# Kernel optimization log

Measured on AMD Instinct MI355X. Metric: run time of the kernel, lower is better.

The kernel has to match this reference:

```python
import jax, jax.numpy as jnp
import numpy as np

D_MODEL = 2048
N_HEADS = 8
N_KV = 4
HEAD_DIM = 256
WINDOW = 1024
EPS = 1e-6
ROPE_BASE = 10000.0


def _rms_norm(x, w):
    # x: [..., D]; matches torch: x * rsqrt(mean(x^2) + eps) * w
    return x * jax.lax.rsqrt(jnp.mean(x * x, axis=-1, keepdims=True) + EPS) * w


def _rope_cos_sin(pos):
    # pos: [T] ints -> cos/sin: [T, HEAD_DIM] (cat(freqs, freqs) as in source)
    inv_freq = 1.0 / (ROPE_BASE ** (jnp.arange(0, HEAD_DIM, 2, dtype=jnp.float32) / HEAD_DIM))
    freqs = pos.astype(jnp.float32)[:, None] * inv_freq[None, :]  # [T, D/2]
    emb = jnp.concatenate([freqs, freqs], axis=-1)                # [T, D]
    return jnp.cos(emb), jnp.sin(emb)


def _apply_rotary(x, cos, sin):
    # x: [B, H, T, D]; interleaved rotate-half exactly as the torch code
    x1 = x[..., 0::2]
    x2 = x[..., 1::2]
    x_rot = jnp.stack([-x2, x1], axis=-1).reshape(x.shape)
    return x * cos[None, None, :, :] + x_rot * sin[None, None, :, :]


def setup_inputs() -> dict:
    key = jax.random.key(0)
    ks = jax.random.split(key, 8)
    B, T = 1, 4096
    s = 0.02
    return {
        "x": jax.random.normal(ks[0], (B, T, D_MODEL), dtype=jnp.float32),
        "pos": jnp.arange(T, dtype=jnp.int32),
        "Wq": jax.random.normal(ks[1], (N_HEADS * HEAD_DIM, D_MODEL), dtype=jnp.float32) * s,
        "Wk": jax.random.normal(ks[2], (N_KV * HEAD_DIM, D_MODEL), dtype=jnp.float32) * s,
        "Wv": jax.random.normal(ks[3], (N_KV * HEAD_DIM, D_MODEL), dtype=jnp.float32) * s,
        "Wo": jax.random.normal(ks[4], (D_MODEL, N_HEADS * HEAD_DIM), dtype=jnp.float32) * s,
        "q_norm_w": jnp.ones((HEAD_DIM,), dtype=jnp.float32),
        "k_norm_w": jnp.ones((HEAD_DIM,), dtype=jnp.float32),
    }


def reference(x, pos, Wq, Wk, Wv, Wo, q_norm_w, k_norm_w):
    B, T, _ = x.shape
    # projections (torch Linear: y = x @ W.T)
    q = (x @ Wq.T).reshape(B, T, N_HEADS, HEAD_DIM).transpose(0, 2, 1, 3)  # [B,H,T,D]
    k = (x @ Wk.T).reshape(B, T, N_KV, HEAD_DIM).transpose(0, 2, 1, 3)    # [B,Hkv,T,D]
    v = (x @ Wv.T).reshape(B, T, N_KV, HEAD_DIM).transpose(0, 2, 1, 3)
    # per-head RMSNorm
    q = _rms_norm(q, q_norm_w)
    k = _rms_norm(k, k_norm_w)
    # RoPE
    cos, sin = _rope_cos_sin(pos)
    q = _apply_rotary(q, cos, sin)
    k = _apply_rotary(k, cos, sin)
    # GQA repeat: [B,Hkv,T,D] -> [B,H,T,D]
    rep = N_HEADS // N_KV
    k = jnp.repeat(k, rep, axis=1)
    v = jnp.repeat(v, rep, axis=1)
    # full scores + sliding-window causal mask (faithful to source)
    scores = jnp.einsum("bhqd,bhkd->bhqk", q, k) / jnp.sqrt(jnp.float32(HEAD_DIM))
    i = jnp.arange(T)[:, None]
    j = jnp.arange(T)[None, :]
    allowed = (j <= i) & (j >= i - WINDOW + 1)  # [T,T]
    scores = jnp.where(allowed[None, None, :, :], scores, -jnp.inf)
    attn = jax.nn.softmax(scores, axis=-1)
    y = jnp.einsum("bhqk,bhkd->bhqd", attn, v)
    y = y.transpose(0, 2, 1, 3).reshape(B, T, N_HEADS * HEAD_DIM)
    return y @ Wo.T
```

## Files before the change

### kernel.cpp

```cpp
#include <hip/hip_runtime.h>
#include <cstdint>
#include <cmath>

typedef __bf16 bf16x8 __attribute__((ext_vector_type(8)));
typedef float  f32x4  __attribute__((ext_vector_type(4)));

#define DEVI __device__ __forceinline__

#define SEQ 4096
#define NH 8
#define NKV 4
#define HD 256
#define WIN 1024

DEVI void gload16(const void* g, void* l) {
  __builtin_amdgcn_global_load_lds((const __attribute__((address_space(1))) void*)g,
                                   (__attribute__((address_space(3))) void*)l,
                                   16, 0, 0);
}

DEVI bf16x8 ld8f(const float* p) {
  const f32x4 a = *(const f32x4*)p;
  const f32x4 b = *(const f32x4*)(p + 4);
  bf16x8 r;
#pragma unroll
  for (int j = 0; j < 4; ++j) { r[j] = (__bf16)a[j]; r[4 + j] = (__bf16)b[j]; }
  return r;
}

DEVI void st1(float* p, float v)  { *p = v; }
DEVI void st1(__bf16* p, float v) { *p = (__bf16)v; }

DEVI void barx() {
  asm volatile("" ::: "memory");
  __builtin_amdgcn_s_barrier();
  asm volatile("" ::: "memory");
}

__global__ __launch_bounds__(256)
void cvt_all(const float* __restrict__ x,  const float* __restrict__ wq,
             const float* __restrict__ wk, const float* __restrict__ wv,
             const float* __restrict__ wo,
             __bf16* __restrict__ xb, __bf16* __restrict__ wqkvb,
             __bf16* __restrict__ wob) {
  const size_t g = (size_t)blockIdx.x * 256 + threadIdx.x;
  const float* src; __bf16* dst; size_t off;
  if      (g < 1048576) { src = x;  dst = xb;               off = g; }
  else if (g < 1572864) { src = wq; dst = wqkvb;            off = g - 1048576; }
  else if (g < 1835008) { src = wk; dst = wqkvb + 4194304;  off = g - 1572864; }
  else if (g < 2097152) { src = wv; dst = wqkvb + 6291456;  off = g - 1835008; }
  else                  { src = wo; dst = wob;              off = g - 2097152; }
  *(bf16x8*)(dst + off * 8) = ld8f(src + off * 8);
}

template <int BM, typename TC>
__global__ __launch_bounds__(512, 2)
void gemm256(const __bf16* __restrict__ A, const __bf16* __restrict__ B,
             TC* __restrict__ C, int N, int K) {
  constexpr int AI    = BM / 128;
  constexpr int MF    = BM / 32;
  constexpr int MH    = MF / 2;
  constexpr int AUNIT = BM * 64;
  constexpr int ASZ   = 4 * AUNIT;
  constexpr int VMC   = 2 * AI + 4;
  __shared__ char lds[ASZ + 65536];

  const int tid  = threadIdx.x;
  const int lane = tid & 63;
  const int wave = tid >> 6;
  const int l15  = lane & 15;
  const int l4   = lane >> 4;
  const int wm   = wave >> 2;
  const int wn   = wave & 3;

  constexpr int nTm = 4096 / BM;
  const int lin  = blockIdx.x;
  const int xcd  = lin & 7;
  const int kk   = lin >> 3;
  const int nTn  = N >> 8;
  const int rowT = kk % nTm;
  const int colT = xcd * (nTn >> 3) + kk / nTm;
  const int row0 = rowT * BM;
  const int col0 = colT << 8;

  const int srow = tid >> 2;
  const int scol = ((tid & 3) ^ ((tid >> 3) & 3)) << 3;
  const __bf16* Asrc = A + (size_t)(row0 + srow) * K + scol;
  const __bf16* Bsrc = B + (size_t)(col0 + srow) * K + scol;

  const int swz  = (l4 ^ ((l15 >> 1) & 3)) << 4;
  const int aoff = (wm * (BM / 2) + l15) * 64 + swz;
  const int boff = ((wn << 6) + l15) * 64 + swz;

  auto stA = [&](int kx, int h) {
    int k0 = kx << 6; if (k0 >= K) k0 = 0;
    const __bf16* s = Asrc + k0 + (h << 5);
    char* d = lds + ((kx & 1) * 2 + h) * AUNIT + wave * 1024;
#pragma unroll
    for (int i = 0; i < AI; ++i)
      gload16(s + (size_t)(i << 7) * K, d + i * 8192);
  };
  auto stB = [&](int kx, int h) {
    int k0 = kx << 6; if (k0 >= K) k0 = 0;
    const __bf16* s = Bsrc + k0 + (h << 5);
    char* d = lds + ASZ + ((kx & 1) * 2 + h) * 16384 + wave * 1024;
#pragma unroll
    for (int i = 0; i < 2; ++i)
      gload16(s + (size_t)(i << 7) * K, d + i * 8192);
  };

  f32x4 acc[MF][4] = {};

  stA(0, 0); stB(0, 0); stA(0, 1); stB(0, 1); stA(1, 0); stB(1, 0);
  asm volatile("s_waitcnt vmcnt(%0)" :: "i"(VMC) : "memory");
  barx();

  const int NT = K >> 6;
  for (int kt = 0; kt < NT; ++kt) {
    const int bb = (kt & 1) * 2;
    bf16x8 bfr[4];
    bf16x8 af[MH];

    auto rd = [&](int h, int mg, bool readB) {
      const char* pa = lds + (bb + h) * AUNIT + aoff;
#pragma unroll
      for (int m = 0; m < MH; ++m)
        af[m] = *(const bf16x8*)(pa + ((mg * MH + m) << 10));
      if (readB) {
        const char* pb = lds + ASZ + (bb + h) * 16384 + boff;
#pragma unroll
        for (int n = 0; n < 4; ++n)
          bfr[n] = *(const bf16x8*)(pb + (n << 10));
      }
    };
    auto mm = [&](int mg) {
      barx();
      __builtin_amdgcn_s_setprio(1);
#pragma unroll
      for (int m = 0; m < MH; ++m)
#pragma unroll
        for (int n = 0; n < 4; ++n)
          acc[mg * MH + m][n] =
              __builtin_amdgcn_mfma_f32_16x16x32_bf16(af[m], bfr[n], acc[mg * MH + m][n], 0, 0, 0);
      __builtin_amdgcn_s_setprio(0);
    };

    rd(0, 0, true);
    stA(kt + 1, 1);
    mm(0);
    rd(0, 1, false);
    stB(kt + 1, 1);
    asm volatile("s_waitcnt vmcnt(%0)" :: "i"(VMC) : "memory");
    mm(1);
    rd(1, 0, true);
    stA(kt + 2, 0);
    mm(0);
    rd(1, 1, false);
    stB(kt + 2, 0);
    asm volatile("s_waitcnt vmcnt(%0)" :: "i"(VMC) : "memory");
    mm(1);
  }
  asm volatile("s_waitcnt vmcnt(0)" ::: "memory");

#pragma unroll
  for (int mf = 0; mf < MF; ++mf) {
    const int rb = row0 + wm * (BM / 2) + (mf >> 2) * 64 + (mf & 3) * 16 + (l4 << 2);
#pragma unroll
    for (int reg = 0; reg < 4; ++reg) {
      TC* crow = C + (size_t)(rb + reg) * N + col0 + (wn << 6) + l15;
#pragma unroll
      for (int n = 0; n < 4; ++n) st1(crow + (n << 4), acc[mf][n][reg]);
    }
  }
}

template <int BM, typename TC>
__global__ __launch_bounds__(512, 2)
void gemm2ph(const __bf16* __restrict__ A, const __bf16* __restrict__ B,
             TC* __restrict__ C, int N, int K) {
  constexpr int AI    = BM / 128;
  constexpr int MF    = BM / 32;
  constexpr int AUNIT = BM * 64;
  constexpr int ASZ   = 4 * AUNIT;
  constexpr int VMC   = 2 * (AI + 2);
  __shared__ char lds[ASZ + 65536];

  const int tid  = threadIdx.x;
  const int lane = tid & 63;
  const int wave = tid >> 6;
  const int l15  = lane & 15;
  const int l4   = lane >> 4;
  const int wm   = wave >> 2;
  const int wn   = wave & 3;

  constexpr int nTm = 4096 / BM;
  const int lin  = blockIdx.x;
  const int xcd  = lin & 7;
  const int kk   = lin >> 3;
  const int nTn  = N >> 8;
  const int rowT = kk % nTm;
  const int colT = xcd * (nTn >> 3) + kk / nTm;
  const int row0 = rowT * BM;
  const int col0 = colT << 8;

  const int srow = tid >> 2;
  const int scol = ((tid & 3) ^ ((tid >> 3) & 3)) << 3;
  const __bf16* Asrc = A + (size_t)(row0 + srow) * K + scol;
  const __bf16* Bsrc = B + (size_t)(col0 + srow) * K + scol;

  const int swz  = (l4 ^ ((l15 >> 1) & 3)) << 4;
  const int aoff = (wm * (BM / 2) + l15) * 64 + swz;
  const int boff = ((wn << 6) + l15) * 64 + swz;

  auto stA = [&](int kx, int h, int b) {
    int k0 = kx << 6; if (k0 >= K) k0 = 0;
    const __bf16* s = Asrc + k0 + (h << 5);
    char* d = lds + (b * 2 + h) * AUNIT + wave * 1024;
#pragma unroll
    for (int i = 0; i < AI; ++i)
      gload16(s + (size_t)(i << 7) * K, d + i * 8192);
  };
  auto stB = [&](int kx, int h, int b) {
    int k0 = kx << 6; if (k0 >= K) k0 = 0;
    const __bf16* s = Bsrc + k0 + (h << 5);
    char* d = lds + ASZ + (b * 2 + h) * 16384 + wave * 1024;
#pragma unroll
    for (int i = 0; i < 2; ++i)
      gload16(s + (size_t)(i << 7) * K, d + i * 8192);
  };

  f32x4 acc[MF][4] = {};

  stA(0, 0, 0); stB(0, 0, 0);
  stA(0, 1, 0); stB(0, 1, 0);
  stA(1, 0, 1); stB(1, 0, 1);

  const int NT = K >> 6;
  for (int kt = 0; kt < NT; ++kt) {
    const int b = kt & 1, nb = b ^ 1;
#pragma unroll
    for (int half = 0; half < 2; ++half) {
      asm volatile("s_waitcnt vmcnt(%0)" :: "i"(VMC) : "memory");
      barx();
      bf16x8 af[4], ag[4], bfr[4];
      const char* pa = lds + (b * 2 + half) * AUNIT + aoff;
      const char* pb = lds + ASZ + (b * 2 + half) * 16384 + boff;
#pragma unroll
      for (int m = 0; m < 4; ++m) af[m] = *(const bf16x8*)(pa + (m << 10));
#pragma unroll
      for (int n = 0; n < 4; ++n) bfr[n] = *(const bf16x8*)(pb + (n << 10));
      if constexpr (BM == 256) {
#pragma unroll
        for (int m = 0; m < 4; ++m) ag[m] = *(const bf16x8*)(pa + 4096 + (m << 10));
      }
      if (half == 0) { stA(kt + 1, 1, nb); stB(kt + 1, 1, nb); }
      else           { stA(kt + 2, 0, b);  stB(kt + 2, 0, b);  }
      __builtin_amdgcn_s_setprio(1);
#pragma unroll
      for (int m = 0; m < 4; ++m)
#pragma unroll
        for (int n = 0; n < 4; ++n)
          acc[m][n] = __builtin_amdgcn_mfma_f32_16x16x32_bf16(af[m], bfr[n], acc[m][n], 0, 0, 0);
      if constexpr (BM == 256) {
#pragma unroll
        for (int m = 0; m < 4; ++m)
#pragma unroll
          for (int n = 0; n < 4; ++n)
            acc[4 + m][n] = __builtin_amdgcn_mfma_f32_16x16x32_bf16(ag[m], bfr[n], acc[4 + m][n], 0, 0, 0);
      }
      __builtin_amdgcn_s_setprio(0);
    }
  }

#pragma unroll
  for (int mf = 0; mf < MF; ++mf) {
    const int rb = row0 + wm * (BM / 2) + (mf >> 2) * 64 + (mf & 3) * 16 + (l4 << 2);
#pragma unroll
    for (int reg = 0; reg < 4; ++reg) {
      TC* crow = C + (size_t)(rb + reg) * N + col0 + (wn << 6) + l15;
#pragma unroll
      for (int n = 0; n < 4; ++n) st1(crow + (n << 4), acc[mf][n][reg]);
    }
  }
}

__global__ __launch_bounds__(256)
void norm_rope_tv(__bf16* __restrict__ qkv, __bf16* __restrict__ Vt,
                  const float* __restrict__ qw, const float* __restrict__ kw,
                  const int* __restrict__ pos) {
  if (blockIdx.x < 12288) {
    const int gw   = blockIdx.x * 4 + (threadIdx.x >> 6);
    const int lane = threadIdx.x & 63;
    __bf16* base; const float* w; int t;
    if (gw < SEQ * NH) {
      t = gw >> 3;
      base = qkv + (size_t)t * 4096 + (gw & 7) * HD;
      w = qw;
    } else {
      const int g = gw - SEQ * NH;
      t = g >> 2;
      base = qkv + (size_t)t * 4096 + 2048 + (g & 3) * HD;
      w = kw;
    }

    const int d0 = lane * 4;
    float v[4]; float ss = 0.f;
#pragma unroll
    for (int j = 0; j < 4; ++j) { v[j] = (float)base[d0 + j]; ss += v[j] * v[j]; }
#pragma unroll
    for (int off = 1; off < 64; off <<= 1) ss += __shfl_xor(ss, off);
    const float rms = rsqrtf(ss * (1.0f / 256.0f) + 1e-6f);
    const float p = (float)pos[t];

    float n[4];
#pragma unroll
    for (int j = 0; j < 4; ++j) n[j] = v[j] * rms * w[d0 + j];

    float outv[4];
#pragma unroll
    for (int e = 0; e < 4; e += 2) {
      const int i0 = d0 + e, i1 = i0 + 1;
      const float f0 = exp2f(-(float)(i0 & 127) * 0.103810253f);
      const float f1 = exp2f(-(float)(i1 & 127) * 0.103810253f);
      float s0, cc0, s1, cc1;
      sincosf(p * f0, &s0, &cc0);
      sincosf(p * f1, &s1, &cc1);
      outv[e]     = n[e] * cc0 - n[e + 1] * s0;
      outv[e + 1] = n[e + 1] * cc1 + n[e] * s1;
    }
#pragma unroll
    for (int j = 0; j < 4; ++j) base[d0 + j] = (__bf16)outv[j];
  } else {
    __shared__ __bf16 tile[64][72];
    const int b   = blockIdx.x - 12288;
    const int tid = threadIdx.x;
    const int tb  = (b & 63) * 64;
    const int yy  = b >> 6;
    const int kvh = yy >> 2;
    const int db  = (yy & 3) * 64;
#pragma unroll
    for (int i = 0; i < 2; ++i) {
      const int s = i * 256 + tid;
      const int r = s >> 3, c = (s & 7) * 8;
      bf16x8 val = *(const bf16x8*)(qkv + (size_t)(tb + r) * 4096 + 3072 + kvh * HD + db + c);
#pragma unroll
      for (int j = 0; j < 8; ++j) tile[r][c + j] = val[j];
    }
    __syncthreads();
#pragma unroll
    for (int i = 0; i < 2; ++i) {
      const int s = i * 256 + tid;
      const int r = s >> 3, c = (s & 7) * 8;
      bf16x8 outv;
#pragma unroll
      for (int j = 0; j < 8; ++j) outv[j] = tile[c + j][r];
      *(bf16x8*)(Vt + (size_t)(kvh * HD + db + r) * SEQ + tb + c) = outv;
    }
  }
}

__global__ __launch_bounds__(256, 2)
void attn_fwd(const __bf16* __restrict__ qkv, const __bf16* __restrict__ Vt,
              __bf16* __restrict__ Y) {
  __shared__ char klds[2][16384];
  __shared__ char vlds[2][16384];
  __shared__ __bf16 Ps[4][16][40];
  const int tid  = threadIdx.x;
  const int lane = tid & 63;
  const int wave = tid >> 6;
  const int l15  = lane & 15;
  const int l4   = lane >> 4;
  const int lin  = blockIdx.x;
  const int head = lin & 7;
  const int q0   = (lin >> 3) * 64;
  const int kvh  = head >> 1;
  const int qw   = q0 + wave * 16;

  bf16x8 qf[8];
  const __bf16* qrow = qkv + (size_t)(qw + l15) * 4096 + head * HD;
#pragma unroll
  for (int ks = 0; ks < 8; ++ks) {
    bf16x8 t = *(const bf16x8*)(qrow + ks * 32 + l4 * 8);
#pragma unroll
    for (int j = 0; j < 8; ++j) t[j] = (__bf16)((float)t[j] * 0.0625f);
    qf[ks] = t;
  }

  f32x4 o[16] = {};
  float l_run[4] = {0.f, 0.f, 0.f, 0.f};

  int lo = q0 - (WIN - 1); if (lo < 0) lo = 0;
  const int kt0 = lo >> 5;
  const int kt1 = (q0 + 63) >> 5;
  const int kbmax = kt1 << 5;

  const int skey = (tid >> 2) & 31;
  const int sdim = tid >> 2;
  const int sg   = (tid & 3) ^ ((tid >> 3) & 3);
  const int sth  = tid >> 7;

  auto stK = [&](int kt, int b) {
    int kb = kt << 5; if (kb > kbmax) kb = kbmax;
    const __bf16* s = qkv + (size_t)(kb + skey) * 4096 + 2048 + kvh * HD
                          + sth * 32 + sg * 8;
    char* d = klds[b] + wave * 1024;
#pragma unroll
    for (int i = 0; i < 4; ++i)
      gload16(s + i * 64, d + i * 4096);
  };
  auto stV = [&](int kt, int b) {
    int kb = kt << 5; if (kb > kbmax) kb = kbmax;
    const __bf16* s = Vt + ((size_t)kvh * HD + sdim) * SEQ + kb + sg * 8;
    char* d = vlds[b] + wave * 1024;
#pragma unroll
    for (int i = 0; i < 4; ++i)
      gload16(s + (size_t)i * 64 * SEQ, d + i * 4096);
  };

  stK(kt0, 0);     stV(kt0, 0);
  stK(kt0 + 1, 1); stV(kt0 + 1, 1);

  const int rswz = (l4 ^ ((l15 >> 1) & 3)) << 4;

  for (int kt = kt0; kt <= kt1; ++kt) {
    const int p  = (kt - kt0) & 1;
    const int kb = kt << 5;
    asm volatile("s_waitcnt vmcnt(8)" ::: "memory");
    barx();

    const char* kbase = klds[p];
    f32x4 s_acc[2] = {};
    __builtin_amdgcn_s_setprio(1);
#pragma unroll
    for (int kn = 0; kn < 2; ++kn) {
#pragma unroll
      for (int ks = 0; ks < 8; ++ks) {
        bf16x8 kf = *(const bf16x8*)(kbase + (ks * 32 + kn * 16 + l15) * 64 + rswz);
        s_acc[kn] = __builtin_amdgcn_mfma_f32_16x16x32_bf16(qf[ks], kf, s_acc[kn], 0, 0, 0);
      }
    }
    __builtin_amdgcn_s_setprio(0);

    if ((kb + 31 <= qw) && (kb >= qw - 1008)) {
#pragma unroll
      for (int reg = 0; reg < 4; ++reg) {
        const int r = l4 * 4 + reg;
        float ps = 0.f;
#pragma unroll
        for (int kn = 0; kn < 2; ++kn) {
          const float pv = __expf(fminf(s_acc[kn][reg], 34.f) - 34.f);
          ps += pv;
          Ps[wave][r][kn * 16 + l15] = (__bf16)pv;
        }
        l_run[reg] += ps;
      }
    } else {
#pragma unroll
      for (int reg = 0; reg < 4; ++reg) {
        const int r  = l4 * 4 + reg;
        const int qg = qw + r;
        float ps = 0.f;
#pragma unroll
        for (int kn = 0; kn < 2; ++kn) {
          const int kg = kb + kn * 16 + l15;
          const bool ok = (kg <= qg) && (kg > qg - WIN);
          const float pv = ok ? __expf(fminf(s_acc[kn][reg], 34.f) - 34.f) : 0.f;
          ps += pv;
          Ps[wave][r][kn * 16 + l15] = (__bf16)pv;
        }
        l_run[reg] += ps;
      }
    }

    const char* vbase = vlds[p];
    bf16x8 pf = *(const bf16x8*)&Ps[wave][l15][l4 * 8];
    __builtin_amdgcn_s_setprio(1);
#pragma unroll
    for (int dn = 0; dn < 16; ++dn) {
      bf16x8 vf = *(const bf16x8*)(vbase + (dn * 16 + l15) * 64 + rswz);
      o[dn] = __builtin_amdgcn_mfma_f32_16x16x32_bf16(pf, vf, o[dn], 0, 0, 0);
    }
    __builtin_amdgcn_s_setprio(0);

    barx();
    stK(kt + 2, p);
    stV(kt + 2, p);
  }
  asm volatile("s_waitcnt vmcnt(0)" ::: "memory");

#pragma unroll
  for (int reg = 0; reg < 4; ++reg) {
#pragma unroll
    for (int off = 1; off < 16; off <<= 1)
      l_run[reg] += __shfl_xor(l_run[reg], off);
    const float inv = 1.0f / l_run[reg];
    const int q = qw + l4 * 4 + reg;
    __bf16* yrow = Y + ((size_t)q * NH + head) * HD + l15;
#pragma unroll
    for (int dn = 0; dn < 16; ++dn)
      yrow[dn * 16] = (__bf16)(o[dn][reg] * inv);
  }
}

extern "C" void kernel_launch(void* const* d_in, const int* in_sizes, int n_in,
                              void* d_out, int out_size, void* d_ws, size_t ws_size,
                              hipStream_t stream) {
  (void)in_sizes; (void)n_in; (void)out_size; (void)ws_size;
  const float* x   = (const float*)d_in[0];
  const int*   pos = (const int*)d_in[1];
  const float* Wq  = (const float*)d_in[2];
  const float* Wk  = (const float*)d_in[3];
  const float* Wv  = (const float*)d_in[4];
  const float* Wo  = (const float*)d_in[5];
  const float* qw  = (const float*)d_in[6];
  const float* kw  = (const float*)d_in[7];
  float* out = (float*)d_out;

  char* ws = (char*)d_ws;
  const size_t MB = 1024 * 1024;
  __bf16* qkv_ws = (__bf16*)(ws);
  __bf16* vt_ws  = (__bf16*)(ws + 32 * MB);
  __bf16* y_ws   = (__bf16*)(ws + 40 * MB);
  __bf16* xb     = (__bf16*)(ws + 56 * MB);
  __bf16* wqkvb  = (__bf16*)(ws + 72 * MB);
  __bf16* wob    = (__bf16*)(ws + 88 * MB);

  cvt_all<<<dim3(10240), dim3(256), 0, stream>>>(x, Wq, Wk, Wv, Wo, xb, wqkvb, wob);
  gemm256<256, __bf16><<<dim3(256), dim3(512), 0, stream>>>(xb, wqkvb, qkv_ws, 4096, 2048);
  norm_rope_tv<<<dim3(13312), dim3(256), 0, stream>>>(qkv_ws, vt_ws, qw, kw, pos);
  attn_fwd<<<dim3(512), dim3(256), 0, stream>>>(qkv_ws, vt_ws, y_ws);
  gemm2ph<128, float><<<dim3(256), dim3(512), 0, stream>>>(y_ws, wob, out, 2048, 2048);
}
```

Measured before the change: 305.8 us.

## Enlarge attention blocks to 128 queries with 8 waves and triple-buffered KV

The attention kernel now runs 512 threads per block, each covering 128 query rows. This halves the grid and lets every K/V tile loaded into LDS serve twice as many queries. The double-buffered K/V staging becomes a three-slot ring, where the next-next tile is issued right after the single barrier, which removes the second per-iteration barrier. The trade-offs are lower occupancy (1 block per CU), more LDS, more masked work per block, and only 256 blocks to spread across the CUs.

Measured after the change: 328.2 us. +7.3%, slower.

```diff
diff --git a/kernel.cpp b/kernel.cpp
--- a/kernel.cpp
+++ b/kernel.cpp
@@ -359,12 +359,12 @@
   }
 }
 
-__global__ __launch_bounds__(256, 2)
+__global__ __launch_bounds__(512, 1)
 void attn_fwd(const __bf16* __restrict__ qkv, const __bf16* __restrict__ Vt,
               __bf16* __restrict__ Y) {
-  __shared__ char klds[2][16384];
-  __shared__ char vlds[2][16384];
-  __shared__ __bf16 Ps[4][16][40];
+  __shared__ char klds[3][16384];
+  __shared__ char vlds[3][16384];
+  __shared__ __bf16 Ps[8][16][40];
   const int tid  = threadIdx.x;
   const int lane = tid & 63;
   const int wave = tid >> 6;
@@ -372,7 +372,7 @@
   const int l4   = lane >> 4;
   const int lin  = blockIdx.x;
   const int head = lin & 7;
-  const int q0   = (lin >> 3) * 64;
+  const int q0   = (lin >> 3) * 128;
   const int kvh  = head >> 1;
   const int qw   = q0 + wave * 16;
 
@@ -391,44 +391,47 @@
 
   int lo = q0 - (WIN - 1); if (lo < 0) lo = 0;
   const int kt0 = lo >> 5;
-  const int kt1 = (q0 + 63) >> 5;
+  const int kt1 = (q0 + 127) >> 5;
   const int kbmax = kt1 << 5;
 
   const int skey = (tid >> 2) & 31;
   const int sdim = tid >> 2;
   const int sg   = (tid & 3) ^ ((tid >> 3) & 3);
-  const int sth  = tid >> 7;
-
-  auto stK = [&](int kt, int b) {
+  const int sks  = tid >> 7;
+
+  auto stK = [&](int kt, char* d) {
     int kb = kt << 5; if (kb > kbmax) kb = kbmax;
     const __bf16* s = qkv + (size_t)(kb + skey) * 4096 + 2048 + kvh * HD
-                          + sth * 32 + sg * 8;
-    char* d = klds[b] + wave * 1024;
-#pragma unroll
-    for (int i = 0; i < 4; ++i)
-      gload16(s + i * 64, d + i * 4096);
+                          + sks * 32 + sg * 8;
+#pragma unroll
+    for (int i = 0; i < 2; ++i)
+      gload16(s + i * 128, d + tid * 16 + i * 8192);
   };
-  auto stV = [&](int kt, int b) {
+  auto stV = [&](int kt, char* d) {
     int kb = kt << 5; if (kb > kbmax) kb = kbmax;
     const __bf16* s = Vt + ((size_t)kvh * HD + sdim) * SEQ + kb + sg * 8;
-    char* d = vlds[b] + wave * 1024;
-#pragma unroll
-    for (int i = 0; i < 4; ++i)
-      gload16(s + (size_t)i * 64 * SEQ, d + i * 4096);
+#pragma unroll
+    for (int i = 0; i < 2; ++i)
+      gload16(s + (size_t)i * 128 * SEQ, d + tid * 16 + i * 8192);
   };
 
-  stK(kt0, 0);     stV(kt0, 0);
-  stK(kt0 + 1, 1); stV(kt0 + 1, 1);
+  stK(kt0, klds[0]);     stV(kt0, vlds[0]);
+  stK(kt0 + 1, klds[1]); stV(kt0 + 1, vlds[1]);
 
   const int rswz = (l4 ^ ((l15 >> 1) & 3)) << 4;
 
+  int rs = 0;
   for (int kt = kt0; kt <= kt1; ++kt) {
-    const int p  = (kt - kt0) & 1;
     const int kb = kt << 5;
-    asm volatile("s_waitcnt vmcnt(8)" ::: "memory");
+    const int ws = (rs == 0) ? 2 : rs - 1;
+
+    asm volatile("s_waitcnt vmcnt(4)" ::: "memory");
     barx();
 
-    const char* kbase = klds[p];
+    stK(kt + 2, klds[ws]);
+    stV(kt + 2, vlds[ws]);
+
+    const char* kbase = klds[rs];
     f32x4 s_acc[2] = {};
     __builtin_amdgcn_s_setprio(1);
 #pragma unroll
@@ -472,7 +475,7 @@
       }
     }
 
-    const char* vbase = vlds[p];
+    const char* vbase = vlds[rs];
     bf16x8 pf = *(const bf16x8*)&Ps[wave][l15][l4 * 8];
     __builtin_amdgcn_s_setprio(1);
 #pragma unroll
@@ -482,9 +485,7 @@
     }
     __builtin_amdgcn_s_setprio(0);
 
-    barx();
-    stK(kt + 2, p);
-    stV(kt + 2, p);
+    rs = (rs == 2) ? 0 : rs + 1;
   }
   asm volatile("s_waitcnt vmcnt(0)" ::: "memory");
 
@@ -528,6 +529,6 @@
   cvt_all<<<dim3(10240), dim3(256), 0, stream>>>(x, Wq, Wk, Wv, Wo, xb, wqkvb, wob);
   gemm256<256, __bf16><<<dim3(256), dim3(512), 0, stream>>>(xb, wqkvb, qkv_ws, 4096, 2048);
   norm_rope_tv<<<dim3(13312), dim3(256), 0, stream>>>(qkv_ws, vt_ws, qw, kw, pos);
-  attn_fwd<<<dim3(512), dim3(256), 0, stream>>>(qkv_ws, vt_ws, y_ws);
+  attn_fwd<<<dim3(256), dim3(512), 0, stream>>>(qkv_ws, vt_ws, y_ws);
   gemm2ph<128, float><<<dim3(256), dim3(512), 0, stream>>>(y_ws, wob, out, 2048, 2048);
 }
```

## Fuse per-head RMSNorm and RoPE into QKV GEMM epilogue

Applied to the files above, without the earlier changes.

The QKV projection GEMM now applies the per-head RMSNorm and rotary embedding directly in its epilogue for Q and K column tiles. Each 256-wide tile is one head, so the sum of squares is reduced across waves through LDS. The separate norm/rope pass, which re-read and re-wrote Q and K in global memory, is removed, leaving a standalone V transpose kernel. The trade is extra epilogue work, LDS barriers and sincos calls inside the GEMM, which may add register pressure and tail latency.

After: 350.3 us. 14.5% more time.

```diff
diff --git a/kernel.cpp b/kernel.cpp
--- a/kernel.cpp
+++ b/kernel.cpp
@@ -53,16 +53,16 @@
   *(bf16x8*)(dst + off * 8) = ld8f(src + off * 8);
 }
 
-template <int BM, typename TC>
 __global__ __launch_bounds__(512, 2)
-void gemm256(const __bf16* __restrict__ A, const __bf16* __restrict__ B,
-             TC* __restrict__ C, int N, int K) {
-  constexpr int AI    = BM / 128;
-  constexpr int MF    = BM / 32;
-  constexpr int MH    = MF / 2;
-  constexpr int AUNIT = BM * 64;
+void gemm_qkv(const __bf16* __restrict__ A, const __bf16* __restrict__ B,
+              __bf16* __restrict__ C, const float* __restrict__ qnw,
+              const float* __restrict__ knw, const int* __restrict__ pos,
+              int N, int K) {
+  constexpr int MF    = 8;
+  constexpr int MH    = 4;
+  constexpr int AUNIT = 16384;
   constexpr int ASZ   = 4 * AUNIT;
-  constexpr int VMC   = 2 * AI + 4;
+  constexpr int VMC   = 8;
   __shared__ char lds[ASZ + 65536];
 
   const int tid  = threadIdx.x;
@@ -73,14 +73,13 @@
   const int wm   = wave >> 2;
   const int wn   = wave & 3;
 
-  constexpr int nTm = 4096 / BM;
   const int lin  = blockIdx.x;
   const int xcd  = lin & 7;
   const int kk   = lin >> 3;
   const int nTn  = N >> 8;
-  const int rowT = kk % nTm;
-  const int colT = xcd * (nTn >> 3) + kk / nTm;
-  const int row0 = rowT * BM;
+  const int rowT = kk % 16;
+  const int colT = xcd * (nTn >> 3) + kk / 16;
+  const int row0 = rowT * 256;
   const int col0 = colT << 8;
 
   const int srow = tid >> 2;
@@ -89,7 +88,7 @@
   const __bf16* Bsrc = B + (size_t)(col0 + srow) * K + scol;
 
   const int swz  = (l4 ^ ((l15 >> 1) & 3)) << 4;
-  const int aoff = (wm * (BM / 2) + l15) * 64 + swz;
+  const int aoff = (wm * 128 + l15) * 64 + swz;
   const int boff = ((wn << 6) + l15) * 64 + swz;
 
   auto stA = [&](int kx, int h) {
@@ -97,7 +96,7 @@
     const __bf16* s = Asrc + k0 + (h << 5);
     char* d = lds + ((kx & 1) * 2 + h) * AUNIT + wave * 1024;
 #pragma unroll
-    for (int i = 0; i < AI; ++i)
+    for (int i = 0; i < 2; ++i)
       gload16(s + (size_t)(i << 7) * K, d + i * 8192);
   };
   auto stB = [&](int kx, int h) {
@@ -162,14 +161,64 @@
   }
   asm volatile("s_waitcnt vmcnt(0)" ::: "memory");
 
-#pragma unroll
-  for (int mf = 0; mf < MF; ++mf) {
-    const int rb = row0 + wm * (BM / 2) + (mf >> 2) * 64 + (mf & 3) * 16 + (l4 << 2);
-#pragma unroll
-    for (int reg = 0; reg < 4; ++reg) {
-      TC* crow = C + (size_t)(rb + reg) * N + col0 + (wn << 6) + l15;
-#pragma unroll
-      for (int n = 0; n < 4; ++n) st1(crow + (n << 4), acc[mf][n][reg]);
+  if (colT < 12) {
+    barx();
+    float* ssb = (float*)lds;
+#pragma unroll
+    for (int mf = 0; mf < MF; ++mf) {
+#pragma unroll
+      for (int reg = 0; reg < 4; ++reg) {
+        float q = 0.f;
+#pragma unroll
+        for (int n = 0; n < 4; ++n) { const float v = acc[mf][n][reg]; q += v * v; }
+        q += __shfl_xor(q, 1); q += __shfl_xor(q, 2);
+        q += __shfl_xor(q, 4); q += __shfl_xor(q, 8);
+        if (l15 == 0) {
+          const int lr = wm * 128 + (mf >> 2) * 64 + (mf & 3) * 16 + (l4 << 2) + reg;
+          ssb[lr * 4 + wn] = q;
+        }
+      }
+    }
+    barx();
+    const float* w = (colT < 8) ? qnw : knw;
+    float wv4[4], fr4[4];
+#pragma unroll
+    for (int n = 0; n < 4; ++n) {
+      const int d = (wn << 6) + n * 16 + l15;
+      wv4[n] = w[d];
+      fr4[n] = exp2f(-(float)(d & 127) * 0.103810253f);
+    }
+    const float sgn = (l15 & 1) ? 1.f : -1.f;
+#pragma unroll
+    for (int mf = 0; mf < MF; ++mf) {
+#pragma unroll
+      for (int reg = 0; reg < 4; ++reg) {
+        const int lr = wm * 128 + (mf >> 2) * 64 + (mf & 3) * 16 + (l4 << 2) + reg;
+        const float ss = ssb[lr * 4 + 0] + ssb[lr * 4 + 1]
+                       + ssb[lr * 4 + 2] + ssb[lr * 4 + 3];
+        const float rms = rsqrtf(ss * (1.0f / 256.0f) + 1e-6f);
+        const float p = (float)pos[row0 + lr];
+        __bf16* crow = C + (size_t)(row0 + lr) * N + col0 + (wn << 6) + l15;
+#pragma unroll
+        for (int n = 0; n < 4; ++n) {
+          const float nv = acc[mf][n][reg] * rms * wv4[n];
+          const float pk = __shfl_xor(nv, 1);
+          float s, c;
+          sincosf(p * fr4[n], &s, &c);
+          crow[n * 16] = (__bf16)(nv * c + sgn * pk * s);
+        }
+      }
+    }
+  } else {
+#pragma unroll
+    for (int mf = 0; mf < MF; ++mf) {
+      const int rb = row0 + wm * 128 + (mf >> 2) * 64 + (mf & 3) * 16 + (l4 << 2);
+#pragma unroll
+      for (int reg = 0; reg < 4; ++reg) {
+        __bf16* crow = C + (size_t)(rb + reg) * N + col0 + (wn << 6) + l15;
+#pragma unroll
+        for (int n = 0; n < 4; ++n) crow[n << 4] = (__bf16)acc[mf][n][reg];
+      }
     }
   }
 }
@@ -285,77 +334,31 @@
 }
 
 __global__ __launch_bounds__(256)
-void norm_rope_tv(__bf16* __restrict__ qkv, __bf16* __restrict__ Vt,
-                  const float* __restrict__ qw, const float* __restrict__ kw,
-                  const int* __restrict__ pos) {
-  if (blockIdx.x < 12288) {
-    const int gw   = blockIdx.x * 4 + (threadIdx.x >> 6);
-    const int lane = threadIdx.x & 63;
-    __bf16* base; const float* w; int t;
-    if (gw < SEQ * NH) {
-      t = gw >> 3;
-      base = qkv + (size_t)t * 4096 + (gw & 7) * HD;
-      w = qw;
-    } else {
-      const int g = gw - SEQ * NH;
-      t = g >> 2;
-      base = qkv + (size_t)t * 4096 + 2048 + (g & 3) * HD;
-      w = kw;
-    }
-
-    const int d0 = lane * 4;
-    float v[4]; float ss = 0.f;
-#pragma unroll
-    for (int j = 0; j < 4; ++j) { v[j] = (float)base[d0 + j]; ss += v[j] * v[j]; }
-#pragma unroll
-    for (int off = 1; off < 64; off <<= 1) ss += __shfl_xor(ss, off);
-    const float rms = rsqrtf(ss * (1.0f / 256.0f) + 1e-6f);
-    const float p = (float)pos[t];
-
-    float n[4];
-#pragma unroll
-    for (int j = 0; j < 4; ++j) n[j] = v[j] * rms * w[d0 + j];
-
-    float outv[4];
-#pragma unroll
-    for (int e = 0; e < 4; e += 2) {
-      const int i0 = d0 + e, i1 = i0 + 1;
-      const float f0 = exp2f(-(float)(i0 & 127) * 0.103810253f);
-      const float f1 = exp2f(-(float)(i1 & 127) * 0.103810253f);
-      float s0, cc0, s1, cc1;
-      sincosf(p * f0, &s0, &cc0);
-      sincosf(p * f1, &s1, &cc1);
-      outv[e]     = n[e] * cc0 - n[e + 1] * s0;
-      outv[e + 1] = n[e + 1] * cc1 + n[e] * s1;
-    }
-#pragma unroll
-    for (int j = 0; j < 4; ++j) base[d0 + j] = (__bf16)outv[j];
-  } else {
-    __shared__ __bf16 tile[64][72];
-    const int b   = blockIdx.x - 12288;
-    const int tid = threadIdx.x;
-    const int tb  = (b & 63) * 64;
-    const int yy  = b >> 6;
-    const int kvh = yy >> 2;
-    const int db  = (yy & 3) * 64;
-#pragma unroll
-    for (int i = 0; i < 2; ++i) {
-      const int s = i * 256 + tid;
-      const int r = s >> 3, c = (s & 7) * 8;
-      bf16x8 val = *(const bf16x8*)(qkv + (size_t)(tb + r) * 4096 + 3072 + kvh * HD + db + c);
-#pragma unroll
-      for (int j = 0; j < 8; ++j) tile[r][c + j] = val[j];
-    }
-    __syncthreads();
-#pragma unroll
-    for (int i = 0; i < 2; ++i) {
-      const int s = i * 256 + tid;
-      const int r = s >> 3, c = (s & 7) * 8;
-      bf16x8 outv;
-#pragma unroll
-      for (int j = 0; j < 8; ++j) outv[j] = tile[c + j][r];
-      *(bf16x8*)(Vt + (size_t)(kvh * HD + db + r) * SEQ + tb + c) = outv;
-    }
+void v_transpose(const __bf16* __restrict__ qkv, __bf16* __restrict__ Vt) {
+  __shared__ __bf16 tile[64][72];
+  const int b   = blockIdx.x;
+  const int tid = threadIdx.x;
+  const int tb  = (b & 63) * 64;
+  const int yy  = b >> 6;
+  const int kvh = yy >> 2;
+  const int db  = (yy & 3) * 64;
+#pragma unroll
+  for (int i = 0; i < 2; ++i) {
+    const int s = i * 256 + tid;
+    const int r = s >> 3, c = (s & 7) * 8;
+    bf16x8 val = *(const bf16x8*)(qkv + (size_t)(tb + r) * 4096 + 3072 + kvh * HD + db + c);
+#pragma unroll
+    for (int j = 0; j < 8; ++j) tile[r][c + j] = val[j];
+  }
+  __syncthreads();
+#pragma unroll
+  for (int i = 0; i < 2; ++i) {
+    const int s = i * 256 + tid;
+    const int r = s >> 3, c = (s & 7) * 8;
+    bf16x8 outv;
+#pragma unroll
+    for (int j = 0; j < 8; ++j) outv[j] = tile[c + j][r];
+    *(bf16x8*)(Vt + (size_t)(kvh * HD + db + r) * SEQ + tb + c) = outv;
   }
 }
 
@@ -526,8 +529,8 @@
   __bf16* wob    = (__bf16*)(ws + 88 * MB);
 
   cvt_all<<<dim3(10240), dim3(256), 0, stream>>>(x, Wq, Wk, Wv, Wo, xb, wqkvb, wob);
-  gemm256<256, __bf16><<<dim3(256), dim3(512), 0, stream>>>(xb, wqkvb, qkv_ws, 4096, 2048);
-  norm_rope_tv<<<dim3(13312), dim3(256), 0, stream>>>(qkv_ws, vt_ws, qw, kw, pos);
+  gemm_qkv<<<dim3(256), dim3(512), 0, stream>>>(xb, wqkvb, qkv_ws, qw, kw, pos, 4096, 2048);
+  v_transpose<<<dim3(1024), dim3(256), 0, stream>>>(qkv_ws, vt_ws);
   attn_fwd<<<dim3(512), dim3(256), 0, stream>>>(qkv_ws, vt_ws, y_ws);
   gemm2ph<128, float><<<dim3(256), dim3(512), 0, stream>>>(y_ws, wob, out, 2048, 2048);
 }
```
